# Kernel optimization log

Hardware: AMD Instinct MI355X
Metric: run time of the kernel (lower is better)

The kernel has to match this reference:

```python
import jax, jax.numpy as jnp
import numpy as np

B, V, E = 1024, 50257, 128

def setup_inputs() -> dict:
    key = jax.random.key(0)
    k1, k2, k3, k4 = jax.random.split(key, 4)
    # xs: one-hot focus-word vectors [B, V]
    focus_ids = jax.random.randint(k1, (B,), 0, V)
    xs = jnp.zeros((B, V), dtype=jnp.float32).at[jnp.arange(B), focus_ids].set(1.0)
    metric = jax.random.normal(k2, (E, E), dtype=jnp.float32)
    EMBEDM = jax.random.normal(k3, (V, E), dtype=jnp.float32)
    NEGEMBEDM = jax.random.normal(k4, (V, E), dtype=jnp.float32)
    return {"xs": xs, "metric": metric, "EMBEDM": EMBEDM, "NEGEMBEDM": NEGEMBEDM}

def reference(xs, metric, EMBEDM, NEGEMBEDM):
    # xs @ EMBEDM : one-hot matmul == row gather, but kept as GEMM to match original math
    xsembeds = xs @ EMBEDM                              # [B, E]
    # dots(vs, ws, metric) = (vs @ metric) @ ws.T
    scores = (xsembeds @ metric) @ NEGEMBEDM.T          # [B, V]
    return jax.nn.log_softmax(scores, axis=1)
```

## Files before the change

### kernel.cpp

```cpp
#include <hip/hip_runtime.h>
#include <hip/hip_bf16.h>
#include <math.h>

#define B_ROWS 1024
#define V_COLS 50257
#define E_DIM  128
#define BM     128
#define BN     128
#define NNB    393
#define VPAD   (NNB * BN)
#define N4     (V_COLS * E_DIM / 4)
#define N4P    (VPAD * E_DIM / 4)

typedef __attribute__((ext_vector_type(8))) short short8;
typedef __attribute__((ext_vector_type(4))) float floatx4;

static __device__ __forceinline__ unsigned short f2bf(float x) {
    union { float f; unsigned int u; } c; c.f = x;
    unsigned int u = c.u;
    unsigned int r = u + 0x7fffu + ((u >> 16) & 1u);
    return (unsigned short)(r >> 16);
}

__global__ void find_idx_kernel(const float4* __restrict__ xs4, int* __restrict__ idx) {
    long i = (long)blockIdx.x * blockDim.x + threadIdx.x;
    const long n4 = (long)B_ROWS * V_COLS / 4;
    if (i >= n4) return;
    float4 v = xs4[i];
    float vals[4] = {v.x, v.y, v.z, v.w};
    #pragma unroll
    for (int c = 0; c < 4; ++c) {
        if (vals[c] != 0.0f) {
            long f = 4 * i + c;
            int b = (int)(f / V_COLS);
            idx[b] = (int)(f - (long)b * V_COLS);
        }
    }
}

__global__ void cvt_bf16_kernel(const float4* __restrict__ src, ushort4* __restrict__ dst) {
    int i = blockIdx.x * blockDim.x + threadIdx.x;
    if (i >= N4P) return;
    ushort4 o;
    if (i < N4) {
        float4 v = src[i];
        o.x = f2bf(v.x); o.y = f2bf(v.y); o.z = f2bf(v.z); o.w = f2bf(v.w);
    } else {
        o.x = 0; o.y = 0; o.z = 0; o.w = 0;
    }
    dst[i] = o;
}

__global__ void compute_t_kernel(const float* __restrict__ EMB, const float* __restrict__ metric,
                                 const int* __restrict__ idx, unsigned short* __restrict__ t) {
    __shared__ float erow[E_DIM];
    int b = blockIdx.x, tid = threadIdx.x;
    int id = idx[b];
    erow[tid] = EMB[(long)id * E_DIM + tid];
    __syncthreads();
    float acc = 0.f;
    #pragma unroll 16
    for (int k = 0; k < E_DIM; ++k) acc += erow[k] * metric[k * E_DIM + tid];
    t[b * E_DIM + tid] = f2bf(acc);
}

template <bool WRITE_OUT>
__global__ __launch_bounds__(256) void gemm_kernel(const unsigned short* __restrict__ t,
                                                   const unsigned short* __restrict__ neg,
                                                   float2* __restrict__ partials,
                                                   const float* __restrict__ lse,
                                                   float* __restrict__ out) {
    __shared__ __align__(16) unsigned char smem[128 * 132 * 4];
    __shared__ float2 stats[2][128];
    __shared__ float lsev[128];

    const int tid  = threadIdx.x;
    const int lane = tid & 63, wave = tid >> 6;
    const int l16  = lane & 15, q = lane >> 4;
    const int wm   = wave >> 1, wn = wave & 1;
    const int mbase = blockIdx.y * BM;
    const int nbase = blockIdx.x * BN;

    if (WRITE_OUT && tid < 128) lsev[tid] = lse[mbase + tid];

    uint4* ldsA = (uint4*)smem;
    uint4* ldsB = (uint4*)(smem + 32768);
    const uint4* srcA = (const uint4*)(t + (size_t)mbase * E_DIM);
    const uint4* srcB = (const uint4*)(neg + (size_t)nbase * E_DIM);
    #pragma unroll
    for (int it = 0; it < 8; ++it) {
        int idx = it * 256 + tid;
        int r = idx >> 4, c = idx & 15;
        int d = (r << 4) + (c ^ (r & 15));
        ldsA[d] = srcA[idx];
        ldsB[d] = srcB[idx];
    }
    __syncthreads();

    floatx4 acc[4][4];
    #pragma unroll
    for (int i = 0; i < 4; ++i)
        #pragma unroll
        for (int j = 0; j < 4; ++j) acc[i][j] = (floatx4){0, 0, 0, 0};

    #pragma unroll
    for (int ks = 0; ks < 4; ++ks) {
        short8 af[4], bfr[4];
        #pragma unroll
        for (int mf = 0; mf < 4; ++mf) {
            int row = wm * 64 + mf * 16 + l16;
            af[mf] = *(const short8*)&ldsA[(row << 4) + ((ks * 4 + q) ^ (row & 15))];
        }
        #pragma unroll
        for (int nt = 0; nt < 4; ++nt) {
            int row = wn * 64 + nt * 16 + l16;
            bfr[nt] = *(const short8*)&ldsB[(row << 4) + ((ks * 4 + q) ^ (row & 15))];
        }
        #pragma unroll
        for (int mf = 0; mf < 4; ++mf)
            #pragma unroll
            for (int nt = 0; nt < 4; ++nt)
                acc[mf][nt] = __builtin_amdgcn_mfma_f32_16x16x32_bf16(af[mf], bfr[nt], acc[mf][nt], 0, 0, 0);
    }


    if (!WRITE_OUT) {
        #pragma unroll
        for (int mf = 0; mf < 4; ++mf) {
            #pragma unroll
            for (int r = 0; r < 4; ++r) {
                bool valid[4];
                #pragma unroll
                for (int nt = 0; nt < 4; ++nt)
                    valid[nt] = (nbase + wn * 64 + nt * 16 + l16) < V_COLS;
                float mx = -INFINITY;
                #pragma unroll
                for (int nt = 0; nt < 4; ++nt)
                    if (valid[nt]) mx = fmaxf(mx, acc[mf][nt][r]);
                #pragma unroll
                for (int d = 1; d < 16; d <<= 1) mx = fmaxf(mx, __shfl_xor(mx, d, 16));
                float s = 0.f;
                #pragma unroll
                for (int nt = 0; nt < 4; ++nt)
                    if (valid[nt]) s += __expf(acc[mf][nt][r] - mx);
                #pragma unroll
                for (int d = 1; d < 16; d <<= 1) s += __shfl_xor(s, d, 16);
                if (l16 == 0) stats[wn][wm * 64 + mf * 16 + q * 4 + r] = make_float2(mx, s);
            }
        }
        __syncthreads();
        if (tid < 128) {
            float2 p0 = stats[0][tid], p1 = stats[1][tid];
            float mm = fmaxf(p0.x, p1.x);
            float ss = p0.y * __expf(p0.x - mm) + p1.y * __expf(p1.x - mm);
            partials[(long)(mbase + tid) * NNB + blockIdx.x] = make_float2(mm, ss);
        }
    } else {
        __syncthreads();
        float* sbuf = (float*)smem;
        #pragma unroll
        for (int mf = 0; mf < 4; ++mf)
            #pragma unroll
            for (int nt = 0; nt < 4; ++nt)
                #pragma unroll
                for (int r = 0; r < 4; ++r)
                    sbuf[(wm * 64 + mf * 16 + q * 4 + r) * 132 + wn * 64 + nt * 16 + l16] = acc[mf][nt][r];
        __syncthreads();
        #pragma unroll 4
        for (int it = 0; it < 64; ++it) {
            int i = it * 256 + tid;
            int r = i >> 7, c = i & 127;
            int col = nbase + c;
            if (col < V_COLS)
                out[(size_t)(mbase + r) * V_COLS + col] = sbuf[r * 132 + c] - lsev[r];
        }
    }
}

__global__ void merge_lse_kernel(const float2* __restrict__ partials, float* __restrict__ lse) {
    int b = blockIdx.x;
    int tid = threadIdx.x;
    float m = -INFINITY, s = 0.f;
    for (int i = tid; i < NNB; i += 256) {
        float2 p = partials[(long)b * NNB + i];
        if (p.x > m) { s = s * __expf(m - p.x) + p.y; m = p.x; }
        else         { s += p.y * __expf(p.x - m); }
    }
    __shared__ float sm[256], ss[256];
    sm[tid] = m; ss[tid] = s;
    __syncthreads();
    for (int off = 128; off > 0; off >>= 1) {
        if (tid < off) {
            float m1 = sm[tid], s1 = ss[tid];
            float m2 = sm[tid + off], s2 = ss[tid + off];
            float mm = fmaxf(m1, m2);
            sm[tid] = mm;
            ss[tid] = s1 * __expf(m1 - mm) + s2 * __expf(m2 - mm);
        }
        __syncthreads();
    }
    if (tid == 0) lse[b] = sm[0] + __logf(ss[0]);
}

extern "C" void kernel_launch(void* const* d_in, const int* in_sizes, int n_in,
                              void* d_out, int out_size, void* d_ws, size_t ws_size,
                              hipStream_t stream) {
    const float* xs     = (const float*)d_in[0];
    const float* metric = (const float*)d_in[1];
    const float* EMB    = (const float*)d_in[2];
    const float* NEG    = (const float*)d_in[3];
    float* out = (float*)d_out;

    char* ws = (char*)d_ws;
    int*            idx      = (int*)ws;
    unsigned short* t        = (unsigned short*)(ws + 4096);
    unsigned short* neg16    = (unsigned short*)(ws + 266240);
    float2*         partials = (float2*)(ws + 13144064);
    float*          lse      = (float*)(ws + 16363520);

    {
        long n4 = (long)B_ROWS * V_COLS / 4;
        int blocks = (int)((n4 + 255) / 256);
        find_idx_kernel<<<blocks, 256, 0, stream>>>((const float4*)xs, idx);
    }
    cvt_bf16_kernel<<<(N4P + 255) / 256, 256, 0, stream>>>((const float4*)NEG, (ushort4*)neg16);
    compute_t_kernel<<<B_ROWS, E_DIM, 0, stream>>>(EMB, metric, idx, t);
    gemm_kernel<false><<<dim3(NNB, B_ROWS / BM), 256, 0, stream>>>(t, neg16, partials, nullptr, nullptr);
    merge_lse_kernel<<<B_ROWS, 256, 0, stream>>>(partials, lse);
    gemm_kernel<true><<<dim3(NNB, B_ROWS / BM), 256, 0, stream>>>(t, neg16, partials, lse, out);
}
```

Baseline: 467.0 us.

## Use nontemporal memory ops, direct LDS loads, and 8-wave GEMM blocks

Input streaming reads and output writes switch to nontemporal loads/stores to avoid cache pollution on the large one-hot matrix and log-prob output. The GEMM tile loads use global_load_lds to write directly into LDS with the swizzle moved to the source address. Blocks grow to 512 threads (4x2 wave layout) and the grid is transposed so consecutive blocks share the same NEG tile. These aim to reduce bandwidth waste and improve latency hiding, at the risk of register/LDS occupancy changes.

```diff
diff --git a/kernel.cpp b/kernel.cpp
--- a/kernel.cpp
+++ b/kernel.cpp
@@ -22,11 +22,18 @@
     return (unsigned short)(r >> 16);
 }
 
-__global__ void find_idx_kernel(const float4* __restrict__ xs4, int* __restrict__ idx) {
+static __device__ __forceinline__ void gload16(const void* g, void* l) {
+    __builtin_amdgcn_global_load_lds(
+        (const __attribute__((address_space(1))) void*)g,
+        (__attribute__((address_space(3))) void*)l,
+        16, 0, 0);
+}
+
+__global__ void find_idx_kernel(const float* __restrict__ xs, int* __restrict__ idx) {
     long i = (long)blockIdx.x * blockDim.x + threadIdx.x;
     const long n4 = (long)B_ROWS * V_COLS / 4;
     if (i >= n4) return;
-    float4 v = xs4[i];
+    floatx4 v = __builtin_nontemporal_load((const floatx4*)xs + i);
     float vals[4] = {v.x, v.y, v.z, v.w};
     #pragma unroll
     for (int c = 0; c < 4; ++c) {
@@ -38,12 +45,12 @@
     }
 }
 
-__global__ void cvt_bf16_kernel(const float4* __restrict__ src, ushort4* __restrict__ dst) {
+__global__ void cvt_bf16_kernel(const float* __restrict__ src, ushort4* __restrict__ dst) {
     int i = blockIdx.x * blockDim.x + threadIdx.x;
     if (i >= N4P) return;
     ushort4 o;
     if (i < N4) {
-        float4 v = src[i];
+        floatx4 v = __builtin_nontemporal_load((const floatx4*)src + i);
         o.x = f2bf(v.x); o.y = f2bf(v.y); o.z = f2bf(v.z); o.w = f2bf(v.w);
     } else {
         o.x = 0; o.y = 0; o.z = 0; o.w = 0;
@@ -65,21 +72,21 @@
 }
 
 template <bool WRITE_OUT>
-__global__ __launch_bounds__(256) void gemm_kernel(const unsigned short* __restrict__ t,
-                                                   const unsigned short* __restrict__ neg,
-                                                   float2* __restrict__ partials,
-                                                   const float* __restrict__ lse,
-                                                   float* __restrict__ out) {
+__global__ __launch_bounds__(512, 4) void gemm_kernel(const unsigned short* __restrict__ t,
+                                                      const unsigned short* __restrict__ neg,
+                                                      float2* __restrict__ partials,
+                                                      const float* __restrict__ lse,
+                                                      float* __restrict__ out) {
     __shared__ __align__(16) unsigned char smem[128 * 132 * 4];
-    __shared__ float2 stats[2][128];
+    __shared__ float2 stats[4][128];
     __shared__ float lsev[128];
 
     const int tid  = threadIdx.x;
     const int lane = tid & 63, wave = tid >> 6;
     const int l16  = lane & 15, q = lane >> 4;
-    const int wm   = wave >> 1, wn = wave & 1;
-    const int mbase = blockIdx.y * BM;
-    const int nbase = blockIdx.x * BN;
+    const int wm   = wave >> 2, wn = wave & 3;
+    const int mbase = blockIdx.x * BM;
+    const int nbase = blockIdx.y * BN;
 
     if (WRITE_OUT && tid < 128) lsev[tid] = lse[mbase + tid];
 
@@ -87,62 +94,62 @@
     uint4* ldsB = (uint4*)(smem + 32768);
     const uint4* srcA = (const uint4*)(t + (size_t)mbase * E_DIM);
     const uint4* srcB = (const uint4*)(neg + (size_t)nbase * E_DIM);
-    #pragma unroll
-    for (int it = 0; it < 8; ++it) {
-        int idx = it * 256 + tid;
-        int r = idx >> 4, c = idx & 15;
-        int d = (r << 4) + (c ^ (r & 15));
-        ldsA[d] = srcA[idx];
-        ldsB[d] = srcB[idx];
+    {
+        const int p0 = wave * 256 + lane;
+        #pragma unroll
+        for (int i = 0; i < 4; ++i) {
+            int p = p0 + i * 64;
+            int r = p >> 4, c = p & 15;
+            int s = (r << 4) + (c ^ (r & 15));
+            int pbase = wave * 256 + i * 64;
+            gload16(srcA + s, ldsA + pbase);
+            gload16(srcB + s, ldsB + pbase);
+        }
     }
     __syncthreads();
 
-    floatx4 acc[4][4];
+    floatx4 acc[4][2];
     #pragma unroll
     for (int i = 0; i < 4; ++i)
         #pragma unroll
-        for (int j = 0; j < 4; ++j) acc[i][j] = (floatx4){0, 0, 0, 0};
+        for (int j = 0; j < 2; ++j) acc[i][j] = (floatx4){0, 0, 0, 0};
 
     #pragma unroll
     for (int ks = 0; ks < 4; ++ks) {
-        short8 af[4], bfr[4];
+        short8 af[4], bfr[2];
         #pragma unroll
         for (int mf = 0; mf < 4; ++mf) {
             int row = wm * 64 + mf * 16 + l16;
             af[mf] = *(const short8*)&ldsA[(row << 4) + ((ks * 4 + q) ^ (row & 15))];
         }
         #pragma unroll
-        for (int nt = 0; nt < 4; ++nt) {
-            int row = wn * 64 + nt * 16 + l16;
-            bfr[nt] = *(const short8*)&ldsB[(row << 4) + ((ks * 4 + q) ^ (row & 15))];
+        for (int nf = 0; nf < 2; ++nf) {
+            int row = wn * 32 + nf * 16 + l16;
+            bfr[nf] = *(const short8*)&ldsB[(row << 4) + ((ks * 4 + q) ^ (row & 15))];
         }
         #pragma unroll
         for (int mf = 0; mf < 4; ++mf)
             #pragma unroll
-            for (int nt = 0; nt < 4; ++nt)
-                acc[mf][nt] = __builtin_amdgcn_mfma_f32_16x16x32_bf16(af[mf], bfr[nt], acc[mf][nt], 0, 0, 0);
+            for (int nf = 0; nf < 2; ++nf)
+                acc[mf][nf] = __builtin_amdgcn_mfma_f32_16x16x32_bf16(af[mf], bfr[nf], acc[mf][nf], 0, 0, 0);
     }
 
 
     if (!WRITE_OUT) {
+        const bool v0 = (nbase + wn * 32 + l16) < V_COLS;
+        const bool v1 = (nbase + wn * 32 + 16 + l16) < V_COLS;
         #pragma unroll
         for (int mf = 0; mf < 4; ++mf) {
             #pragma unroll
             for (int r = 0; r < 4; ++r) {
-                bool valid[4];
-                #pragma unroll
-                for (int nt = 0; nt < 4; ++nt)
-                    valid[nt] = (nbase + wn * 64 + nt * 16 + l16) < V_COLS;
                 float mx = -INFINITY;
-                #pragma unroll
-                for (int nt = 0; nt < 4; ++nt)
-                    if (valid[nt]) mx = fmaxf(mx, acc[mf][nt][r]);
+                if (v0) mx = acc[mf][0][r];
+                if (v1) mx = fmaxf(mx, acc[mf][1][r]);
                 #pragma unroll
                 for (int d = 1; d < 16; d <<= 1) mx = fmaxf(mx, __shfl_xor(mx, d, 16));
                 float s = 0.f;
-                #pragma unroll
-                for (int nt = 0; nt < 4; ++nt)
-                    if (valid[nt]) s += __expf(acc[mf][nt][r] - mx);
+                if (v0) s += __expf(acc[mf][0][r] - mx);
+                if (v1) s += __expf(acc[mf][1][r] - mx);
                 #pragma unroll
                 for (int d = 1; d < 16; d <<= 1) s += __shfl_xor(s, d, 16);
                 if (l16 == 0) stats[wn][wm * 64 + mf * 16 + q * 4 + r] = make_float2(mx, s);
@@ -150,10 +157,11 @@
         }
         __syncthreads();
         if (tid < 128) {
-            float2 p0 = stats[0][tid], p1 = stats[1][tid];
-            float mm = fmaxf(p0.x, p1.x);
-            float ss = p0.y * __expf(p0.x - mm) + p1.y * __expf(p1.x - mm);
-            partials[(long)(mbase + tid) * NNB + blockIdx.x] = make_float2(mm, ss);
+            float2 p0 = stats[0][tid], p1 = stats[1][tid], p2 = stats[2][tid], p3 = stats[3][tid];
+            float mm = fmaxf(fmaxf(p0.x, p1.x), fmaxf(p2.x, p3.x));
+            float ss = p0.y * __expf(p0.x - mm) + p1.y * __expf(p1.x - mm)
+                     + p2.y * __expf(p2.x - mm) + p3.y * __expf(p3.x - mm);
+            partials[(long)(mbase + tid) * NNB + blockIdx.y] = make_float2(mm, ss);
         }
     } else {
         __syncthreads();
@@ -161,18 +169,19 @@
         #pragma unroll
         for (int mf = 0; mf < 4; ++mf)
             #pragma unroll
-            for (int nt = 0; nt < 4; ++nt)
+            for (int nf = 0; nf < 2; ++nf)
                 #pragma unroll
                 for (int r = 0; r < 4; ++r)
-                    sbuf[(wm * 64 + mf * 16 + q * 4 + r) * 132 + wn * 64 + nt * 16 + l16] = acc[mf][nt][r];
+                    sbuf[(wm * 64 + mf * 16 + q * 4 + r) * 132 + wn * 32 + nf * 16 + l16] = acc[mf][nf][r];
         __syncthreads();
         #pragma unroll 4
-        for (int it = 0; it < 64; ++it) {
-            int i = it * 256 + tid;
+        for (int it = 0; it < 32; ++it) {
+            int i = it * 512 + tid;
             int r = i >> 7, c = i & 127;
             int col = nbase + c;
             if (col < V_COLS)
-                out[(size_t)(mbase + r) * V_COLS + col] = sbuf[r * 132 + c] - lsev[r];
+                __builtin_nontemporal_store(sbuf[r * 132 + c] - lsev[r],
+                                            &out[(size_t)(mbase + r) * V_COLS + col]);
         }
     }
 }
@@ -221,11 +230,11 @@
     {
         long n4 = (long)B_ROWS * V_COLS / 4;
         int blocks = (int)((n4 + 255) / 256);
-        find_idx_kernel<<<blocks, 256, 0, stream>>>((const float4*)xs, idx);
-    }
-    cvt_bf16_kernel<<<(N4P + 255) / 256, 256, 0, stream>>>((const float4*)NEG, (ushort4*)neg16);
+        find_idx_kernel<<<blocks, 256, 0, stream>>>(xs, idx);
+    }
+    cvt_bf16_kernel<<<(N4P + 255) / 256, 256, 0, stream>>>(NEG, (ushort4*)neg16);
     compute_t_kernel<<<B_ROWS, E_DIM, 0, stream>>>(EMB, metric, idx, t);
-    gemm_kernel<false><<<dim3(NNB, B_ROWS / BM), 256, 0, stream>>>(t, neg16, partials, nullptr, nullptr);
+    gemm_kernel<false><<<dim3(B_ROWS / BM, NNB), 512, 0, stream>>>(t, neg16, partials, nullptr, nullptr);
     merge_lse_kernel<<<B_ROWS, 256, 0, stream>>>(partials, lse);
-    gemm_kernel<true><<<dim3(NNB, B_ROWS / BM), 256, 0, stream>>>(t, neg16, partials, lse, out);
-}
+    gemm_kernel<true><<<dim3(B_ROWS / BM, NNB), 512, 0, stream>>>(t, neg16, partials, lse, out);
+}
```

Result: no change. 474.2 us (+1.5%).
